# Kernel tuning notes

Hardware: AMD Instinct MI355X
Metric: run time of the kernel (lower is better)

## Reference

```python
import jax, jax.numpy as jnp
import numpy as np

B, NBC, H, W, HID, OUT = 4, 128, 64, 64, 64, 1
NINT = H * W

def _lin_init(key, fan_in, fan_out):
    kw, kb = jax.random.split(key)
    bound = 1.0 / np.sqrt(fan_in)
    w = jax.random.uniform(kw, (fan_in, fan_out), minval=-bound, maxval=bound, dtype=jnp.float32)
    b = jax.random.uniform(kb, (fan_out,), minval=-bound, maxval=bound, dtype=jnp.float32)
    return w, b

def setup_inputs() -> dict:
    key = jax.random.key(0)
    ks = jax.random.split(key, 7)
    boundary_info = jax.random.normal(ks[0], (B, NBC, 3), dtype=jnp.float32)
    interior_coords = jax.random.uniform(ks[1], (B, NINT, 2), minval=-1.0, maxval=1.0, dtype=jnp.float32)
    W0, b0 = _lin_init(ks[2], 3, HID)        # boundary_encoder layer 0
    W1, b1 = _lin_init(ks[3], HID, HID)      # boundary_encoder layer 1
    G0w, G0b = _lin_init(ks[4], HID + 2, HID)  # green_kernel layer 0
    G1w, G1b = _lin_init(ks[5], HID, HID)      # green_kernel layer 1
    G2w, G2b = _lin_init(ks[6], HID, OUT)      # green_kernel layer 2
    return {"boundary_info": boundary_info, "interior_coords": interior_coords,
            "W0": W0, "b0": b0, "W1": W1, "b1": b1,
            "G0w": G0w, "G0b": G0b, "G1w": G1w, "G1b": G1b,
            "G2w": G2w, "G2b": G2b,
            "interior_h": H, "interior_w": W}

def reference(boundary_info, interior_coords, W0, b0, W1, b1,
              G0w, G0b, G1w, G1b, G2w, G2b, interior_h, interior_w):
    batch, n_bc, _ = boundary_info.shape
    hid = W0.shape[1]
    # boundary encoder: (B, NBC, HID)
    bf = jax.nn.relu(boundary_info @ W0 + b0)
    bf = jax.nn.relu(bf @ W1 + b1)
    # green kernel layer 0: split weight over concat([bf, coords]) so the
    # concatenated (B,NBC,NINT,HID+2) tensor is never materialized.
    a = bf @ G0w[:hid]                      # (B, NBC, HID)
    c = interior_coords @ G0w[hid:]         # (B, NINT, HID)
    h1 = jax.nn.relu(a[:, :, None, :] + c[:, None, :, :] + G0b)  # (B,NBC,NINT,HID)
    h2 = jax.nn.relu(h1 @ G1w + G1b)        # (B, NBC, NINT, HID)
    contribution = h2 @ G2w + G2b           # (B, NBC, NINT, OUT)
    u = contribution.sum(axis=1) / n_bc     # (B, NINT, OUT)
    return u.reshape(batch, 1, interior_h, interior_w)
```

## Files before the change

kernel.cpp:

```cpp
#include <hip/hip_runtime.h>
#include <hip/hip_bf16.h>

#define BB   4
#define NBC  128
#define NINT 4096
#define HID  64

using short8  = __attribute__((ext_vector_type(8)))  short;
using float16 = __attribute__((ext_vector_type(16))) float;

static __device__ __forceinline__ short f2bf(float f) {
    __hip_bfloat16 h = __float2bfloat16(f);
    return __builtin_bit_cast(short, h);
}

__global__ void __launch_bounds__(64) bge_prep(
    const float* __restrict__ binfo,
    const float* __restrict__ W0,
    const float* __restrict__ b0,
    const float* __restrict__ W1,
    const float* __restrict__ b1,
    const float* __restrict__ G0w,
    const float* __restrict__ G0b,
    float* __restrict__ aprime)
{
    const int row = blockIdx.x;
    const int t   = threadIdx.x;
    __shared__ float sh[HID];

    const float x0 = binfo[row*3+0];
    const float x1 = binfo[row*3+1];
    const float x2 = binfo[row*3+2];

    float h = x0*W0[t] + x1*W0[64+t] + x2*W0[128+t] + b0[t];
    h = fmaxf(h, 0.0f);
    sh[t] = h;
    __syncthreads();

    float acc = b1[t];
    #pragma unroll 8
    for (int k = 0; k < HID; ++k) acc += sh[k] * W1[k*64 + t];
    acc = fmaxf(acc, 0.0f);
    __syncthreads();
    sh[t] = acc;
    __syncthreads();

    float a = G0b[t];
    #pragma unroll 8
    for (int k = 0; k < HID; ++k) a += sh[k] * G0w[k*64 + t];
    aprime[row*HID + t] = a;
}

__global__ void __launch_bounds__(256) bge_main(
    const float* __restrict__ icoord,
    const float* __restrict__ G0w,
    const float* __restrict__ G1w,
    const float* __restrict__ G1b,
    const float* __restrict__ G2w,
    const float* __restrict__ G2b,
    const float* __restrict__ aprime,
    float* __restrict__ out)
{
    __shared__ float ldsA[NBC * HID];
    __shared__ float ldsS[4 * 64 * 16];
    __shared__ float red[32][8];

    const int b    = blockIdx.y;
    const int i0   = blockIdx.x * 32;
    const int tid  = threadIdx.x;
    const int wv   = tid >> 6;
    const int lane = tid & 63;
    const int hf   = lane >> 5;
    const int ln   = lane & 31;

    {
        const float4* src = (const float4*)(aprime + (size_t)b * NBC * HID);
        float4* dst = (float4*)ldsA;
        for (int idx = tid; idx < NBC*HID/4; idx += 256) dst[idx] = src[idx];
    }

    const int i = i0 + ln;
    const float cx = icoord[((size_t)b*NINT + i)*2 + 0];
    const float cy = icoord[((size_t)b*NINT + i)*2 + 1];
    float cre[4][8];
    #pragma unroll
    for (int st = 0; st < 4; ++st)
        #pragma unroll
        for (int jj = 0; jj < 8; ++jj) {
            const int k = st*16 + hf*8 + jj;
            cre[st][jj] = cx*G0w[64*64 + k] + cy*G0w[65*64 + k];
        }

    short8 bfrag[4][2];
    #pragma unroll
    for (int st = 0; st < 4; ++st)
        #pragma unroll
        for (int t = 0; t < 2; ++t)
            #pragma unroll
            for (int jj = 0; jj < 8; ++jj) {
                const int k = st*16 + hf*8 + jj;
                bfrag[st][t][jj] = f2bf(G1w[k*64 + t*32 + ln]);
            }

    const float b1v0 = G1b[ln],      b1v1 = G1b[32 + ln];
    const float g2v0 = G2w[ln],      g2v1 = G2w[32 + ln];
    const float g2bv = G2b[0];

    float16 bias0, bias1;
    #pragma unroll
    for (int r = 0; r < 16; ++r) { bias0[r] = b1v0; bias1[r] = b1v1; }

    float s[16];
    #pragma unroll
    for (int r = 0; r < 16; ++r) s[r] = 0.0f;

    __syncthreads();

    #pragma unroll 2
    for (int bc = wv*32; bc < wv*32 + 32; ++bc) {
        const float* arow = ldsA + bc*HID;
        float16 acc0, acc1;
        #pragma unroll
        for (int st = 0; st < 4; ++st) {
            const float* ap = arow + st*16 + hf*8;
            short8 af;
            #pragma unroll
            for (int jj = 0; jj < 8; ++jj)
                af[jj] = f2bf(fmaxf(ap[jj] + cre[st][jj], 0.0f));
            if (st == 0) {
                acc0 = __builtin_amdgcn_mfma_f32_32x32x16_bf16(af, bfrag[0][0], bias0, 0, 0, 0);
                acc1 = __builtin_amdgcn_mfma_f32_32x32x16_bf16(af, bfrag[0][1], bias1, 0, 0, 0);
            } else {
                acc0 = __builtin_amdgcn_mfma_f32_32x32x16_bf16(af, bfrag[st][0], acc0, 0, 0, 0);
                acc1 = __builtin_amdgcn_mfma_f32_32x32x16_bf16(af, bfrag[st][1], acc1, 0, 0, 0);
            }
        }
        #pragma unroll
        for (int r = 0; r < 16; ++r)
            s[r] += fmaxf(acc0[r], 0.0f)*g2v0 + fmaxf(acc1[r], 0.0f)*g2v1;
    }

    #pragma unroll
    for (int r = 0; r < 16; ++r) ldsS[(wv*64 + lane)*16 + r] = s[r];
    __syncthreads();

    const int m   = tid >> 3;
    const int ch  = tid & 7;
    const int h_m = (m >> 2) & 1;
    const int r_m = (m & 3) | ((m >> 3) << 2);
    float acc = 0.0f;
    #pragma unroll
    for (int W = 0; W < 4; ++W)
        #pragma unroll
        for (int q = 0; q < 4; ++q) {
            const int l = h_m*32 + ch*4 + q;
            acc += ldsS[(W*64 + l)*16 + r_m];
        }
    red[m][ch] = acc;
    __syncthreads();

    if (tid < 32) {
        float tot = 0.0f;
        #pragma unroll
        for (int c2 = 0; c2 < 8; ++c2) tot += red[tid][c2];
        out[(size_t)b*NINT + i0 + tid] = tot * (1.0f/128.0f) + g2bv;
    }
}

extern "C" void kernel_launch(void* const* d_in, const int* in_sizes, int n_in,
                              void* d_out, int out_size, void* d_ws, size_t ws_size,
                              hipStream_t stream) {
    const float* binfo  = (const float*)d_in[0];
    const float* icoord = (const float*)d_in[1];
    const float* W0     = (const float*)d_in[2];
    const float* b0     = (const float*)d_in[3];
    const float* W1     = (const float*)d_in[4];
    const float* b1     = (const float*)d_in[5];
    const float* G0w    = (const float*)d_in[6];
    const float* G0b    = (const float*)d_in[7];
    const float* G1w    = (const float*)d_in[8];
    const float* G1b    = (const float*)d_in[9];
    const float* G2w    = (const float*)d_in[10];
    const float* G2b    = (const float*)d_in[11];

    float* aprime = (float*)d_ws;

    hipLaunchKernelGGL(bge_prep, dim3(BB*NBC), dim3(64), 0, stream,
                       binfo, W0, b0, W1, b1, G0w, G0b, aprime);
    hipLaunchKernelGGL(bge_main, dim3(NINT/32, BB), dim3(256), 0, stream,
                       icoord, G0w, G1w, G1b, G2w, G2b, aprime,
                       (float*)d_out);
}
```

Measured before the change: 118.8 us.

## Widen main kernel to 8 waves, truncate bf16 packing, batch prep rows

The main kernel now runs 512 threads per block, so each wave handles 16 boundary rows instead of 32. The A staging buffer and the reduction scratch share one LDS array, padded to stride 17 to avoid bank conflicts. bf16 conversion becomes a truncating byte-perm pack and the G1 bias is added after the MFMA. The prep kernel processes 4 rows per block with weights cached in LDS. The aim is more latency hiding and fewer conversion instructions, at the cost of truncation instead of round-to-nearest and extra register pressure under the 4-blocks-per-SIMD bound.

```diff
diff --git a/kernel.cpp b/kernel.cpp
--- a/kernel.cpp
+++ b/kernel.cpp
@@ -8,13 +8,21 @@
 
 using short8  = __attribute__((ext_vector_type(8)))  short;
 using float16 = __attribute__((ext_vector_type(16))) float;
+using f2      = __attribute__((ext_vector_type(2)))  float;
+using int4v   = __attribute__((ext_vector_type(4)))  int;
 
 static __device__ __forceinline__ short f2bf(float f) {
     __hip_bfloat16 h = __float2bfloat16(f);
     return __builtin_bit_cast(short, h);
 }
-
-__global__ void __launch_bounds__(64) bge_prep(
+static __device__ __forceinline__ unsigned fbits(float f) {
+    return __builtin_bit_cast(unsigned, f);
+}
+static __device__ __forceinline__ unsigned pack_bf_trunc(float lo, float hi) {
+    return __builtin_amdgcn_perm(fbits(hi), fbits(lo), 0x07060302u);
+}
+
+__global__ void __launch_bounds__(256) bge_prep(
     const float* __restrict__ binfo,
     const float* __restrict__ W0,
     const float* __restrict__ b0,
@@ -24,34 +32,41 @@
     const float* __restrict__ G0b,
     float* __restrict__ aprime)
 {
-    const int row = blockIdx.x;
-    const int t   = threadIdx.x;
-    __shared__ float sh[HID];
+    __shared__ float sW1[HID * HID];
+    __shared__ float sG0[HID * HID];
+    __shared__ float shv [4][HID];
+    __shared__ float shv2[4][HID];
+
+    const int tid = threadIdx.x;
+    const int wv  = tid >> 6;
+    const int t   = tid & 63;
+    const int row = blockIdx.x * 4 + wv;
+
+    for (int idx = tid; idx < HID * HID / 4; idx += 256) {
+        ((float4*)sW1)[idx] = ((const float4*)W1)[idx];
+        ((float4*)sG0)[idx] = ((const float4*)G0w)[idx];
+    }
 
     const float x0 = binfo[row*3+0];
     const float x1 = binfo[row*3+1];
     const float x2 = binfo[row*3+2];
-
-    float h = x0*W0[t] + x1*W0[64+t] + x2*W0[128+t] + b0[t];
-    h = fmaxf(h, 0.0f);
-    sh[t] = h;
+    float h = fmaxf(x0*W0[t] + x1*W0[64+t] + x2*W0[128+t] + b0[t], 0.0f);
+    shv[wv][t] = h;
     __syncthreads();
 
     float acc = b1[t];
     #pragma unroll 8
-    for (int k = 0; k < HID; ++k) acc += sh[k] * W1[k*64 + t];
-    acc = fmaxf(acc, 0.0f);
-    __syncthreads();
-    sh[t] = acc;
+    for (int k = 0; k < HID; ++k) acc += shv[wv][k] * sW1[k*64 + t];
+    shv2[wv][t] = fmaxf(acc, 0.0f);
     __syncthreads();
 
     float a = G0b[t];
     #pragma unroll 8
-    for (int k = 0; k < HID; ++k) a += sh[k] * G0w[k*64 + t];
+    for (int k = 0; k < HID; ++k) a += shv2[wv][k] * sG0[k*64 + t];
     aprime[row*HID + t] = a;
 }
 
-__global__ void __launch_bounds__(256) bge_main(
+__global__ void __launch_bounds__(512, 4) bge_main(
     const float* __restrict__ icoord,
     const float* __restrict__ G0w,
     const float* __restrict__ G1w,
@@ -61,9 +76,10 @@
     const float* __restrict__ aprime,
     float* __restrict__ out)
 {
-    __shared__ float ldsA[NBC * HID];
-    __shared__ float ldsS[4 * 64 * 16];
-    __shared__ float red[32][8];
+    __shared__ __align__(16) float smem[8704 + 512];
+    float* const ldsA = smem;
+    float* const ldsS = smem;
+    float* const red  = smem + 8704;
 
     const int b    = blockIdx.y;
     const int i0   = blockIdx.x * 32;
@@ -76,19 +92,23 @@
     {
         const float4* src = (const float4*)(aprime + (size_t)b * NBC * HID);
         float4* dst = (float4*)ldsA;
-        for (int idx = tid; idx < NBC*HID/4; idx += 256) dst[idx] = src[idx];
+        for (int idx = tid; idx < NBC*HID/4; idx += 512) dst[idx] = src[idx];
     }
 
     const int i = i0 + ln;
     const float cx = icoord[((size_t)b*NINT + i)*2 + 0];
     const float cy = icoord[((size_t)b*NINT + i)*2 + 1];
-    float cre[4][8];
+    float4 cre4[4][2];
     #pragma unroll
     for (int st = 0; st < 4; ++st)
         #pragma unroll
-        for (int jj = 0; jj < 8; ++jj) {
-            const int k = st*16 + hf*8 + jj;
-            cre[st][jj] = cx*G0w[64*64 + k] + cy*G0w[65*64 + k];
+        for (int h = 0; h < 2; ++h) {
+            const int k = st*16 + hf*8 + h*4;
+            cre4[st][h] = make_float4(
+                cx*G0w[64*64 + k+0] + cy*G0w[65*64 + k+0],
+                cx*G0w[64*64 + k+1] + cy*G0w[65*64 + k+1],
+                cx*G0w[64*64 + k+2] + cy*G0w[65*64 + k+2],
+                cx*G0w[64*64 + k+3] + cy*G0w[65*64 + k+3]);
         }
 
     short8 bfrag[4][2];
@@ -102,67 +122,82 @@
                 bfrag[st][t][jj] = f2bf(G1w[k*64 + t*32 + ln]);
             }
 
-    const float b1v0 = G1b[ln],      b1v1 = G1b[32 + ln];
-    const float g2v0 = G2w[ln],      g2v1 = G2w[32 + ln];
+    const float b1v0 = G1b[ln],  b1v1 = G1b[32 + ln];
+    const float g2v0 = G2w[ln],  g2v1 = G2w[32 + ln];
     const float g2bv = G2b[0];
 
-    float16 bias0, bias1;
+    const float16 zc = (float16)0.0f;
+    f2 s2[8];
     #pragma unroll
-    for (int r = 0; r < 16; ++r) { bias0[r] = b1v0; bias1[r] = b1v1; }
-
-    float s[16];
-    #pragma unroll
-    for (int r = 0; r < 16; ++r) s[r] = 0.0f;
+    for (int q = 0; q < 8; ++q) s2[q] = (f2)0.0f;
 
     __syncthreads();
 
     #pragma unroll 2
-    for (int bc = wv*32; bc < wv*32 + 32; ++bc) {
+    for (int bc = wv*16; bc < wv*16 + 16; ++bc) {
         const float* arow = ldsA + bc*HID;
         float16 acc0, acc1;
         #pragma unroll
         for (int st = 0; st < 4; ++st) {
-            const float* ap = arow + st*16 + hf*8;
-            short8 af;
-            #pragma unroll
-            for (int jj = 0; jj < 8; ++jj)
-                af[jj] = f2bf(fmaxf(ap[jj] + cre[st][jj], 0.0f));
+            const float4* ap4 = (const float4*)(arow + st*16 + hf*8);
+            float4 v0 = ap4[0], v1 = ap4[1];
+            const float4 c0 = cre4[st][0], c1 = cre4[st][1];
+            v0.x = fmaxf(v0.x + c0.x, 0.0f); v0.y = fmaxf(v0.y + c0.y, 0.0f);
+            v0.z = fmaxf(v0.z + c0.z, 0.0f); v0.w = fmaxf(v0.w + c0.w, 0.0f);
+            v1.x = fmaxf(v1.x + c1.x, 0.0f); v1.y = fmaxf(v1.y + c1.y, 0.0f);
+            v1.z = fmaxf(v1.z + c1.z, 0.0f); v1.w = fmaxf(v1.w + c1.w, 0.0f);
+            int4v di;
+            di[0] = (int)pack_bf_trunc(v0.x, v0.y);
+            di[1] = (int)pack_bf_trunc(v0.z, v0.w);
+            di[2] = (int)pack_bf_trunc(v1.x, v1.y);
+            di[3] = (int)pack_bf_trunc(v1.z, v1.w);
+            const short8 af = __builtin_bit_cast(short8, di);
             if (st == 0) {
-                acc0 = __builtin_amdgcn_mfma_f32_32x32x16_bf16(af, bfrag[0][0], bias0, 0, 0, 0);
-                acc1 = __builtin_amdgcn_mfma_f32_32x32x16_bf16(af, bfrag[0][1], bias1, 0, 0, 0);
+                acc0 = __builtin_amdgcn_mfma_f32_32x32x16_bf16(af, bfrag[0][0], zc, 0, 0, 0);
+                acc1 = __builtin_amdgcn_mfma_f32_32x32x16_bf16(af, bfrag[0][1], zc, 0, 0, 0);
             } else {
                 acc0 = __builtin_amdgcn_mfma_f32_32x32x16_bf16(af, bfrag[st][0], acc0, 0, 0, 0);
                 acc1 = __builtin_amdgcn_mfma_f32_32x32x16_bf16(af, bfrag[st][1], acc1, 0, 0, 0);
             }
         }
         #pragma unroll
-        for (int r = 0; r < 16; ++r)
-            s[r] += fmaxf(acc0[r], 0.0f)*g2v0 + fmaxf(acc1[r], 0.0f)*g2v1;
-    }
-
-    #pragma unroll
-    for (int r = 0; r < 16; ++r) ldsS[(wv*64 + lane)*16 + r] = s[r];
-    __syncthreads();
-
-    const int m   = tid >> 3;
-    const int ch  = tid & 7;
-    const int h_m = (m >> 2) & 1;
-    const int r_m = (m & 3) | ((m >> 3) << 2);
-    float acc = 0.0f;
-    #pragma unroll
-    for (int W = 0; W < 4; ++W)
-        #pragma unroll
-        for (int q = 0; q < 4; ++q) {
-            const int l = h_m*32 + ch*4 + q;
-            acc += ldsS[(W*64 + l)*16 + r_m];
+        for (int q = 0; q < 8; ++q) {
+            f2 a0; a0[0] = acc0[2*q] + b1v0; a0[1] = acc0[2*q+1] + b1v0;
+            f2 a1; a1[0] = acc1[2*q] + b1v1; a1[1] = acc1[2*q+1] + b1v1;
+            a0[0] = fmaxf(a0[0], 0.0f); a0[1] = fmaxf(a0[1], 0.0f);
+            a1[0] = fmaxf(a1[0], 0.0f); a1[1] = fmaxf(a1[1], 0.0f);
+            s2[q] += a0 * g2v0 + a1 * g2v1;
         }
-    red[m][ch] = acc;
+    }
+
+    __syncthreads();
+
+    {
+        float* base = ldsS + (wv*64 + lane)*17;
+        #pragma unroll
+        for (int q = 0; q < 8; ++q) { base[2*q] = s2[q][0]; base[2*q+1] = s2[q][1]; }
+    }
+    __syncthreads();
+
+    {
+        const int m   = tid >> 4;
+        const int ch  = tid & 15;
+        const int h_m = (m >> 2) & 1;
+        const int r_m = (m & 3) | ((m >> 3) << 2);
+        const int wvr = ch >> 1;
+        const int ln0 = (ch & 1) * 16;
+        float acc = 0.0f;
+        #pragma unroll
+        for (int q = 0; q < 16; ++q)
+            acc += ldsS[(wvr*64 + h_m*32 + ln0 + q)*17 + r_m];
+        red[m*16 + ch] = acc;
+    }
     __syncthreads();
 
     if (tid < 32) {
         float tot = 0.0f;
         #pragma unroll
-        for (int c2 = 0; c2 < 8; ++c2) tot += red[tid][c2];
+        for (int c2 = 0; c2 < 16; ++c2) tot += red[tid*16 + c2];
         out[(size_t)b*NINT + i0 + tid] = tot * (1.0f/128.0f) + g2bv;
     }
 }
@@ -185,9 +220,9 @@
 
     float* aprime = (float*)d_ws;
 
-    hipLaunchKernelGGL(bge_prep, dim3(BB*NBC), dim3(64), 0, stream,
+    hipLaunchKernelGGL(bge_prep, dim3(BB*NBC/4), dim3(256), 0, stream,
                        binfo, W0, b0, W1, b1, G0w, G0b, aprime);
-    hipLaunchKernelGGL(bge_main, dim3(NINT/32, BB), dim3(256), 0, stream,
+    hipLaunchKernelGGL(bge_main, dim3(NINT/32, BB), dim3(512), 0, stream,
                        icoord, G0w, G1w, G1b, G2w, G2b, aprime,
                        (float*)d_out);
 }
```

Result: no change. 117.8 us (-0.8%).
